# Kernel tuning notes

Hardware: AMD Instinct MI355X
Metric: run time of the kernel (lower is better)

## Reference

```python
import jax, jax.numpy as jnp
import numpy as np

N_NODE, N_GRAPH, EMBED_DIM, NUM_HEADS = 512, 16, 768, 12
HEAD_DIM = EMBED_DIM // NUM_HEADS


def setup_inputs() -> dict:
    key = jax.random.key(0)
    ks = jax.random.split(key, 12)
    s = 1.0 / np.sqrt(EMBED_DIM)
    inp = {
        "x": jax.random.normal(ks[0], (N_NODE, N_GRAPH, EMBED_DIM), jnp.float32),
        "attn_bias": jax.random.normal(ks[1], (N_GRAPH, NUM_HEADS, N_NODE, N_NODE), jnp.float32),
        "attn_mask": jnp.zeros((N_NODE, N_NODE), jnp.float32),
        "key_padding_mask": jnp.zeros((N_GRAPH, N_NODE), dtype=bool),
        "wq": jax.random.normal(ks[2], (EMBED_DIM, EMBED_DIM), jnp.float32) * s,
        "bq": jax.random.normal(ks[3], (EMBED_DIM,), jnp.float32) * 0.01,
        "wk": jax.random.normal(ks[4], (EMBED_DIM, EMBED_DIM), jnp.float32) * s,
        "bk": jax.random.normal(ks[5], (EMBED_DIM,), jnp.float32) * 0.01,
        "wv": jax.random.normal(ks[6], (EMBED_DIM, EMBED_DIM), jnp.float32) * s,
        "bv": jax.random.normal(ks[7], (EMBED_DIM,), jnp.float32) * 0.01,
        "wo": jax.random.normal(ks[8], (EMBED_DIM, EMBED_DIM), jnp.float32) * s,
        "bo": jax.random.normal(ks[9], (EMBED_DIM,), jnp.float32) * 0.01,
    }
    return inp


def reference(x, attn_bias, attn_mask, key_padding_mask, wq, bq, wk, bk, wv, bv, wo, bo):
    n_node, n_graph, embed_dim = x.shape
    h, d = NUM_HEADS, HEAD_DIM
    scaling = d ** (-0.5)
    # projections (eqx Linear: x @ W.T + b)
    q = (x @ wq.T + bq) * scaling
    k = x @ wk.T + bk
    v = x @ wv.T + bv
    # (n_node, n_graph*h, d) -> (n_graph*h, n_node, d)
    q = q.reshape(n_node, n_graph * h, d).transpose((1, 0, 2))
    k = k.reshape(n_node, n_graph * h, d).transpose((1, 0, 2))
    v = v.reshape(n_node, n_graph * h, d).transpose((1, 0, 2))
    # (n_graph*h, n_node, n_node)
    attn_weights = jnp.einsum("bqd,bkd->bqk", q, k)
    attn_weights = attn_weights + attn_bias.reshape(n_graph * h, n_node, n_node)
    attn_weights = attn_weights + attn_mask[None, :, :]
    # key padding mask: (n_graph, n_node) -> broadcast over heads and query dim
    pad = key_padding_mask[:, None, None, :]  # (n_graph, 1, 1, n_node)
    attn_weights = attn_weights.reshape(n_graph, h, n_node, n_node)
    attn_weights = jnp.where(pad, float("-inf"), attn_weights)
    attn_weights = attn_weights.reshape(n_graph * h, n_node, n_node)
    attn_probs = jax.nn.softmax(attn_weights.astype(jnp.float32), axis=-1)
    attn = jnp.einsum("bqk,bkd->bqd", attn_probs, v)
    attn = attn.transpose((1, 0, 2)).reshape(n_node, n_graph, embed_dim)
    return attn @ wo.T + bo
```

## Files before the change

### kernel.cpp

```cpp
#include <hip/hip_runtime.h>
#include <cstdint>
#include <cstddef>

#define N_NODE 512
#define N_GRAPH 16
#define EMBED 768
#define NHEAD 12
#define HDIM 64
#define NB (N_GRAPH * NHEAD)
#define MROWS (N_NODE * N_GRAPH)

typedef __attribute__((ext_vector_type(8))) __bf16 bf16x8;
typedef __attribute__((ext_vector_type(4))) float f32x4;
typedef __attribute__((ext_vector_type(4))) unsigned short u16x4;

__device__ inline unsigned short f2bf(float f) {
  unsigned u = __builtin_bit_cast(unsigned, f);
  u += 0x7fff + ((u >> 16) & 1);
  return (unsigned short)(u >> 16);
}

__device__ inline void gload_lds16(const void* g, void* l) {
  __builtin_amdgcn_global_load_lds(
      (const __attribute__((address_space(1))) void*)g,
      (__attribute__((address_space(3))) void*)l, 16, 0, 0);
}

__global__ void cvt_kernel(const float* __restrict__ in,
                           unsigned short* __restrict__ out, int n4) {
  int i = blockIdx.x * blockDim.x + threadIdx.x;
  if (i >= n4) return;
  f32x4 v = reinterpret_cast<const f32x4*>(in)[i];
  u16x4 o;
  o.x = f2bf(v.x); o.y = f2bf(v.y); o.z = f2bf(v.z); o.w = f2bf(v.w);
  reinterpret_cast<u16x4*>(out)[i] = o;
}

__global__ __launch_bounds__(256) void qkv_gemm(
    const unsigned short* __restrict__ xb,
    const unsigned short* __restrict__ wqb, const unsigned short* __restrict__ wkb,
    const unsigned short* __restrict__ wvb,
    const float* __restrict__ bq, const float* __restrict__ bk,
    const float* __restrict__ bv,
    unsigned short* __restrict__ qo, unsigned short* __restrict__ ko,
    unsigned short* __restrict__ vto) {
  __shared__ unsigned short As[128 * 32];
  __shared__ unsigned short Bs[128 * 32];
  const int z = blockIdx.z;
  const unsigned short* W = (z == 0) ? wqb : (z == 1) ? wkb : wvb;
  const float* bias = (z == 0) ? bq : (z == 1) ? bk : bv;
  const int m0 = blockIdx.x * 128, n0 = blockIdx.y * 128;
  const int tid = threadIdx.x;
  const int w = tid >> 6, lane = tid & 63, g = lane >> 4, c = lane & 15;
  const int wm = (w >> 1) * 64, wn = (w & 1) * 64;
  const int t1 = w * 128 + lane, t2 = t1 + 64;
  const unsigned short* a1 = xb + (size_t)(m0 + (t1 >> 2)) * EMBED + (t1 & 3) * 8;
  const unsigned short* a2 = xb + (size_t)(m0 + (t2 >> 2)) * EMBED + (t2 & 3) * 8;
  const unsigned short* b1 = W + (size_t)(n0 + (t1 >> 2)) * EMBED + (t1 & 3) * 8;
  const unsigned short* b2 = W + (size_t)(n0 + (t2 >> 2)) * EMBED + (t2 & 3) * 8;
  char* asb = (char*)As + w * 2048;
  char* bsb = (char*)Bs + w * 2048;
  f32x4 acc[4][4] = {};
  for (int k0 = 0; k0 < EMBED; k0 += 32) {
    gload_lds16(a1 + k0, asb);
    gload_lds16(a2 + k0, asb + 1024);
    gload_lds16(b1 + k0, bsb);
    gload_lds16(b2 + k0, bsb + 1024);
    __syncthreads();
    bf16x8 af[4], bfr[4];
#pragma unroll
    for (int mi = 0; mi < 4; ++mi)
      af[mi] = *reinterpret_cast<const bf16x8*>(&As[(wm + mi * 16 + c) * 32 + g * 8]);
#pragma unroll
    for (int ni = 0; ni < 4; ++ni)
      bfr[ni] = *reinterpret_cast<const bf16x8*>(&Bs[(wn + ni * 16 + c) * 32 + g * 8]);
#pragma unroll
    for (int mi = 0; mi < 4; ++mi)
#pragma unroll
      for (int ni = 0; ni < 4; ++ni)
        acc[mi][ni] = __builtin_amdgcn_mfma_f32_16x16x32_bf16(af[mi], bfr[ni],
                                                              acc[mi][ni], 0, 0, 0);
    __syncthreads();
  }
#pragma unroll
  for (int mi = 0; mi < 4; ++mi) {
#pragma unroll
    for (int ni = 0; ni < 4; ++ni) {
#pragma unroll
      for (int i = 0; i < 4; ++i) {
        int m = m0 + wm + mi * 16 + g * 4 + i;
        int n = n0 + wn + ni * 16 + c;
        float v = acc[mi][ni][i] + bias[n];
        int node = m >> 4, graph = m & 15, head = n >> 6, d = n & 63;
        size_t bidx = (size_t)(graph * NHEAD + head);
        if (z == 0) {
          v *= 0.125f;
          qo[(bidx * N_NODE + node) * HDIM + d] = f2bf(v);
        } else if (z == 1) {
          ko[(bidx * N_NODE + node) * HDIM + d] = f2bf(v);
        } else {
          vto[(bidx * HDIM + d) * N_NODE + node] = f2bf(v);
        }
      }
    }
  }
}

__global__ __launch_bounds__(256) void attn_kernel(
    const unsigned short* __restrict__ qb, const unsigned short* __restrict__ kb,
    const unsigned short* __restrict__ vtb, const float* __restrict__ bias,
    const float* __restrict__ amask, const unsigned char* __restrict__ kpm,
    unsigned short* __restrict__ attn_out) {
  __shared__ unsigned short P[4][16 * 72];
  const int b = blockIdx.y, qt = blockIdx.x;
  const int tid = threadIdx.x;
  const int w = tid >> 6, lane = tid & 63, g = lane >> 4, c = lane & 15;
  const int graph = b / NHEAD, head = b % NHEAD;
  const int qbase = qt * 64 + w * 16;
  const size_t bQ = (size_t)b * N_NODE;
  const unsigned short* qptr = qb + (bQ + qbase + c) * HDIM + g * 8;
  bf16x8 aq0 = *reinterpret_cast<const bf16x8*>(qptr);
  bf16x8 aq1 = *reinterpret_cast<const bf16x8*>(qptr + 32);
  f32x4 o[4] = {};
  float m_run = -INFINITY, l_run = 0.0f;
  const float* bias_row = bias + ((size_t)b * N_NODE + qbase + c) * N_NODE;
  const float* amask_row = amask + (size_t)(qbase + c) * N_NODE;
  const unsigned char* kpm_row = kpm + graph * N_NODE;
  unsigned short* Pw = P[w];
  for (int it = 0; it < 8; ++it) {
    const int kbk = it * 64;
    f32x4 s[4];
#pragma unroll
    for (int kf = 0; kf < 4; ++kf) {
      const unsigned short* kp = kb + (bQ + kbk + kf * 16 + c) * HDIM + g * 8;
      bf16x8 b0 = *reinterpret_cast<const bf16x8*>(kp);
      bf16x8 b1 = *reinterpret_cast<const bf16x8*>(kp + 32);
      f32x4 acc = {};
      acc = __builtin_amdgcn_mfma_f32_16x16x32_bf16(b0, aq0, acc, 0, 0, 0);
      acc = __builtin_amdgcn_mfma_f32_16x16x32_bf16(b1, aq1, acc, 0, 0, 0);
      s[kf] = acc;
    }
#pragma unroll
    for (int kf = 0; kf < 4; ++kf) {
      const int k4 = kbk + kf * 16 + g * 4;
      f32x4 bv4 = *reinterpret_cast<const f32x4*>(bias_row + k4);
      f32x4 mv4 = *reinterpret_cast<const f32x4*>(amask_row + k4);
      unsigned pm4 = *reinterpret_cast<const unsigned*>(kpm_row + k4);
#pragma unroll
      for (int i = 0; i < 4; ++i) {
        float v = s[kf][i] + bv4[i] + mv4[i];
        s[kf][i] = ((pm4 >> (8 * i)) & 0xffu) ? -1e30f : v;
      }
    }
    float mx = s[0][0];
#pragma unroll
    for (int kf = 0; kf < 4; ++kf)
#pragma unroll
      for (int i = 0; i < 4; ++i) mx = fmaxf(mx, s[kf][i]);
    mx = fmaxf(mx, __shfl_xor(mx, 16, 64));
    mx = fmaxf(mx, __shfl_xor(mx, 32, 64));
    const float mn = fmaxf(m_run, mx);
    const float sc = __expf(m_run - mn);
    m_run = mn;
    float rs = 0.0f;
#pragma unroll
    for (int kf = 0; kf < 4; ++kf) {
      u16x4 pw;
#pragma unroll
      for (int i = 0; i < 4; ++i) {
        float p = __expf(s[kf][i] - mn);
        rs += p;
        pw[i] = f2bf(p);
      }
      *reinterpret_cast<u16x4*>(&Pw[c * 72 + kf * 16 + g * 4]) = pw;
    }
    rs += __shfl_xor(rs, 16, 64);
    rs += __shfl_xor(rs, 32, 64);
    l_run = l_run * sc + rs;
    float scq[4];
#pragma unroll
    for (int i = 0; i < 4; ++i) scq[i] = __shfl(sc, (lane >> 4) * 4 + i, 64);
#pragma unroll
    for (int dt = 0; dt < 4; ++dt)
#pragma unroll
      for (int i = 0; i < 4; ++i) o[dt][i] *= scq[i];
    asm volatile("s_waitcnt lgkmcnt(0)" ::: "memory");
#pragma unroll
    for (int kc = 0; kc < 2; ++kc) {
      bf16x8 ap = *reinterpret_cast<const bf16x8*>(&Pw[c * 72 + kc * 32 + g * 8]);
#pragma unroll
      for (int dt = 0; dt < 4; ++dt) {
        const unsigned short* vp =
            vtb + ((size_t)b * HDIM + dt * 16 + c) * N_NODE + kbk + kc * 32 + g * 8;
        bf16x8 bv = *reinterpret_cast<const bf16x8*>(vp);
        o[dt] = __builtin_amdgcn_mfma_f32_16x16x32_bf16(ap, bv, o[dt], 0, 0, 0);
      }
    }
  }
  float invq[4];
#pragma unroll
  for (int i = 0; i < 4; ++i)
    invq[i] = 1.0f / __shfl(l_run, (lane >> 4) * 4 + i, 64);
#pragma unroll
  for (int i = 0; i < 4; ++i) {
    int node = qbase + g * 4 + i;
#pragma unroll
    for (int dt = 0; dt < 4; ++dt) {
      int d = dt * 16 + c;
      attn_out[((size_t)(node * N_GRAPH + graph)) * EMBED + head * HDIM + d] =
          f2bf(o[dt][i] * invq[i]);
    }
  }
}

__global__ __launch_bounds__(256) void oproj_gemm(
    const unsigned short* __restrict__ ab, const unsigned short* __restrict__ wob,
    const float* __restrict__ bo, float* __restrict__ out) {
  __shared__ unsigned short As[128 * 32];
  __shared__ unsigned short Bs[128 * 32];
  const int m0 = blockIdx.x * 128, n0 = blockIdx.y * 128;
  const int tid = threadIdx.x;
  const int w = tid >> 6, lane = tid & 63, g = lane >> 4, c = lane & 15;
  const int wm = (w >> 1) * 64, wn = (w & 1) * 64;
  const int t1 = w * 128 + lane, t2 = t1 + 64;
  const unsigned short* a1 = ab + (size_t)(m0 + (t1 >> 2)) * EMBED + (t1 & 3) * 8;
  const unsigned short* a2 = ab + (size_t)(m0 + (t2 >> 2)) * EMBED + (t2 & 3) * 8;
  const unsigned short* b1 = wob + (size_t)(n0 + (t1 >> 2)) * EMBED + (t1 & 3) * 8;
  const unsigned short* b2 = wob + (size_t)(n0 + (t2 >> 2)) * EMBED + (t2 & 3) * 8;
  char* asb = (char*)As + w * 2048;
  char* bsb = (char*)Bs + w * 2048;
  f32x4 acc[4][4] = {};
  for (int k0 = 0; k0 < EMBED; k0 += 32) {
    gload_lds16(a1 + k0, asb);
    gload_lds16(a2 + k0, asb + 1024);
    gload_lds16(b1 + k0, bsb);
    gload_lds16(b2 + k0, bsb + 1024);
    __syncthreads();
    bf16x8 af[4], bfr[4];
#pragma unroll
    for (int mi = 0; mi < 4; ++mi)
      af[mi] = *reinterpret_cast<const bf16x8*>(&As[(wm + mi * 16 + c) * 32 + g * 8]);
#pragma unroll
    for (int ni = 0; ni < 4; ++ni)
      bfr[ni] = *reinterpret_cast<const bf16x8*>(&Bs[(wn + ni * 16 + c) * 32 + g * 8]);
#pragma unroll
    for (int mi = 0; mi < 4; ++mi)
#pragma unroll
      for (int ni = 0; ni < 4; ++ni)
        acc[mi][ni] = __builtin_amdgcn_mfma_f32_16x16x32_bf16(af[mi], bfr[ni],
                                                              acc[mi][ni], 0, 0, 0);
    __syncthreads();
  }
#pragma unroll
  for (int mi = 0; mi < 4; ++mi) {
#pragma unroll
    for (int ni = 0; ni < 4; ++ni) {
#pragma unroll
      for (int i = 0; i < 4; ++i) {
        int m = m0 + wm + mi * 16 + g * 4 + i;
        int n = n0 + wn + ni * 16 + c;
        out[(size_t)m * EMBED + n] = acc[mi][ni][i] + bo[n];
      }
    }
  }
}

extern "C" void kernel_launch(void* const* d_in, const int* in_sizes, int n_in,
                              void* d_out, int out_size, void* d_ws, size_t ws_size,
                              hipStream_t stream) {
  const float* x = (const float*)d_in[0];
  const float* attn_bias = (const float*)d_in[1];
  const float* attn_mask = (const float*)d_in[2];
  const unsigned char* kpm = (const unsigned char*)d_in[3];
  const float* wq = (const float*)d_in[4];
  const float* bq = (const float*)d_in[5];
  const float* wk = (const float*)d_in[6];
  const float* bk = (const float*)d_in[7];
  const float* wv = (const float*)d_in[8];
  const float* bv = (const float*)d_in[9];
  const float* wo = (const float*)d_in[10];
  const float* bo = (const float*)d_in[11];

  char* ws = (char*)d_ws;
  const size_t xbf_b = (size_t)MROWS * EMBED * 2;
  const size_t wbf_b = (size_t)EMBED * EMBED * 2;
  const size_t qkv_b = (size_t)NB * N_NODE * HDIM * 2;
  unsigned short* x_bf = (unsigned short*)ws;  ws += xbf_b;
  unsigned short* wq_bf = (unsigned short*)ws; ws += wbf_b;
  unsigned short* wk_bf = (unsigned short*)ws; ws += wbf_b;
  unsigned short* wv_bf = (unsigned short*)ws; ws += wbf_b;
  unsigned short* wo_bf = (unsigned short*)ws; ws += wbf_b;
  unsigned short* q_bf = (unsigned short*)ws;  ws += qkv_b;
  unsigned short* k_bf = (unsigned short*)ws;  ws += qkv_b;
  unsigned short* vt_bf = (unsigned short*)ws; ws += qkv_b;
  unsigned short* attn_bf = (unsigned short*)ws;

  const int n4x = MROWS * EMBED / 4;
  const int n4w = EMBED * EMBED / 4;
  cvt_kernel<<<(n4x + 255) / 256, 256, 0, stream>>>(x, x_bf, n4x);
  cvt_kernel<<<(n4w + 255) / 256, 256, 0, stream>>>(wq, wq_bf, n4w);
  cvt_kernel<<<(n4w + 255) / 256, 256, 0, stream>>>(wk, wk_bf, n4w);
  cvt_kernel<<<(n4w + 255) / 256, 256, 0, stream>>>(wv, wv_bf, n4w);
  cvt_kernel<<<(n4w + 255) / 256, 256, 0, stream>>>(wo, wo_bf, n4w);

  qkv_gemm<<<dim3(MROWS / 128, EMBED / 128, 3), 256, 0, stream>>>(
      x_bf, wq_bf, wk_bf, wv_bf, bq, bk, bv, q_bf, k_bf, vt_bf);

  attn_kernel<<<dim3(N_NODE / 64, NB), 256, 0, stream>>>(
      q_bf, k_bf, vt_bf, attn_bias, attn_mask, kpm, attn_bf);

  oproj_gemm<<<dim3(MROWS / 128, EMBED / 128), 256, 0, stream>>>(
      attn_bf, wo_bf, bo, (float*)d_out);
}
```

Before: 536.1 us.

## Software-pipeline K and bias loads across iterations in attention kernel

```diff
diff --git a/kernel.cpp b/kernel.cpp
--- a/kernel.cpp
+++ b/kernel.cpp
@@ -127,29 +127,60 @@
   const float* amask_row = amask + (size_t)(qbase + c) * N_NODE;
   const unsigned char* kpm_row = kpm + graph * N_NODE;
   unsigned short* Pw = P[w];
+
+  bf16x8 kA[2][4], kB[2][4];
+  f32x4 bvp[2][4];
+#pragma unroll
+  for (int kf = 0; kf < 4; ++kf) {
+    const unsigned short* kp = kb + (bQ + kf * 16 + c) * HDIM + g * 8;
+    kA[0][kf] = *reinterpret_cast<const bf16x8*>(kp);
+    kB[0][kf] = *reinterpret_cast<const bf16x8*>(kp + 32);
+    bvp[0][kf] = *reinterpret_cast<const f32x4*>(bias_row + kf * 16 + g * 4);
+  }
+
+#pragma unroll
   for (int it = 0; it < 8; ++it) {
+    const int cur = it & 1, nxt = cur ^ 1;
     const int kbk = it * 64;
-    f32x4 s[4];
-#pragma unroll
-    for (int kf = 0; kf < 4; ++kf) {
-      const unsigned short* kp = kb + (bQ + kbk + kf * 16 + c) * HDIM + g * 8;
-      bf16x8 b0 = *reinterpret_cast<const bf16x8*>(kp);
-      bf16x8 b1 = *reinterpret_cast<const bf16x8*>(kp + 32);
-      f32x4 acc = {};
-      acc = __builtin_amdgcn_mfma_f32_16x16x32_bf16(b0, aq0, acc, 0, 0, 0);
-      acc = __builtin_amdgcn_mfma_f32_16x16x32_bf16(b1, aq1, acc, 0, 0, 0);
-      s[kf] = acc;
-    }
+    bf16x8 vf[2][4];
+#pragma unroll
+    for (int kc = 0; kc < 2; ++kc)
+#pragma unroll
+      for (int dt = 0; dt < 4; ++dt)
+        vf[kc][dt] = *reinterpret_cast<const bf16x8*>(
+            vtb + ((size_t)b * HDIM + dt * 16 + c) * N_NODE + kbk + kc * 32 + g * 8);
+    f32x4 mv[4];
+    unsigned pm4[4];
 #pragma unroll
     for (int kf = 0; kf < 4; ++kf) {
       const int k4 = kbk + kf * 16 + g * 4;
-      f32x4 bv4 = *reinterpret_cast<const f32x4*>(bias_row + k4);
-      f32x4 mv4 = *reinterpret_cast<const f32x4*>(amask_row + k4);
-      unsigned pm4 = *reinterpret_cast<const unsigned*>(kpm_row + k4);
+      mv[kf] = *reinterpret_cast<const f32x4*>(amask_row + k4);
+      pm4[kf] = *reinterpret_cast<const unsigned*>(kpm_row + k4);
+    }
+    f32x4 s[4];
+#pragma unroll
+    for (int kf = 0; kf < 4; ++kf) {
+      f32x4 acc = {};
+      acc = __builtin_amdgcn_mfma_f32_16x16x32_bf16(kA[cur][kf], aq0, acc, 0, 0, 0);
+      acc = __builtin_amdgcn_mfma_f32_16x16x32_bf16(kB[cur][kf], aq1, acc, 0, 0, 0);
+      s[kf] = acc;
+    }
+    if (it < 7) {
+      const int nbk = kbk + 64;
+#pragma unroll
+      for (int kf = 0; kf < 4; ++kf) {
+        const unsigned short* kp = kb + (bQ + nbk + kf * 16 + c) * HDIM + g * 8;
+        kA[nxt][kf] = *reinterpret_cast<const bf16x8*>(kp);
+        kB[nxt][kf] = *reinterpret_cast<const bf16x8*>(kp + 32);
+        bvp[nxt][kf] = *reinterpret_cast<const f32x4*>(bias_row + nbk + kf * 16 + g * 4);
+      }
+    }
+#pragma unroll
+    for (int kf = 0; kf < 4; ++kf) {
 #pragma unroll
       for (int i = 0; i < 4; ++i) {
-        float v = s[kf][i] + bv4[i] + mv4[i];
-        s[kf][i] = ((pm4 >> (8 * i)) & 0xffu) ? -1e30f : v;
+        float v = s[kf][i] + bvp[cur][kf][i] + mv[kf][i];
+        s[kf][i] = ((pm4[kf] >> (8 * i)) & 0xffu) ? -1e30f : v;
       }
     }
     float mx = s[0][0];
@@ -184,17 +215,12 @@
     for (int dt = 0; dt < 4; ++dt)
 #pragma unroll
       for (int i = 0; i < 4; ++i) o[dt][i] *= scq[i];
-    asm volatile("s_waitcnt lgkmcnt(0)" ::: "memory");
 #pragma unroll
     for (int kc = 0; kc < 2; ++kc) {
       bf16x8 ap = *reinterpret_cast<const bf16x8*>(&Pw[c * 72 + kc * 32 + g * 8]);
 #pragma unroll
-      for (int dt = 0; dt < 4; ++dt) {
-        const unsigned short* vp =
-            vtb + ((size_t)b * HDIM + dt * 16 + c) * N_NODE + kbk + kc * 32 + g * 8;
-        bf16x8 bv = *reinterpret_cast<const bf16x8*>(vp);
-        o[dt] = __builtin_amdgcn_mfma_f32_16x16x32_bf16(ap, bv, o[dt], 0, 0, 0);
-      }
+      for (int dt = 0; dt < 4; ++dt)
+        o[dt] = __builtin_amdgcn_mfma_f32_16x16x32_bf16(ap, vf[kc][dt], o[dt], 0, 0, 0);
     }
   }
   float invq[4];
```

New measurement: 536.2 us. No clear change (+0.0%).
